# Performance work log

Hardware: AMD Instinct MI355X
Metric: run time of the kernel (lower is better)

## Reference

```python
import jax, jax.numpy as jnp
import numpy as np

N = 50000      # nodes
E = 800000     # edges (avg degree 16)
IN = 256       # in_ft
F1, F2, F3 = 128, 128, 256  # out_ft_list


def _p(k, shape):
    return jax.random.normal(k, shape, dtype=jnp.float32) * 0.05


def setup_inputs() -> dict:
    key = jax.random.key(0)
    ks = jax.random.split(key, 14)
    return {
        "x": jax.random.normal(ks[0], (N, IN), dtype=jnp.float32),
        "edge_index": jax.random.randint(ks[1], (2, E), 0, N, dtype=jnp.int64),
        # proj Linear
        "Wp": _p(ks[2], (IN, F1)), "bp": jnp.zeros((F1,), jnp.float32),
        # SAGEConv1: lin_l (on aggregated neighbors, carries bias) + lin_r (root)
        "Wl1": _p(ks[3], (IN, F1)), "bl1": jnp.zeros((F1,), jnp.float32), "Wr1": _p(ks[4], (IN, F1)),
        # SAGEConv2: input is concat(x_p, h1) -> 2*F1
        "Wl2": _p(ks[5], (2 * F1, F2)), "bl2": jnp.zeros((F2,), jnp.float32), "Wr2": _p(ks[6], (2 * F1, F2)),
        # SAGEConv3: input is concat(x_p, h1, h2) -> 2*F1 + F2
        "Wl3": _p(ks[7], (2 * F1 + F2, F3)), "bl3": jnp.zeros((F3,), jnp.float32), "Wr3": _p(ks[8], (2 * F1 + F2, F3)),
    }


def _sage_mean(h, src, dst, Wl, bl, Wr):
    # PyG SAGEConv(aggr='mean'): out = lin_l(mean_{j in N(i)} h_j) + lin_r(h_i)
    msg = h[src]                                              # [E, F_in]
    summed = jax.ops.segment_sum(msg, dst, num_segments=N)    # [N, F_in]
    deg = jax.ops.segment_sum(jnp.ones((src.shape[0],), h.dtype), dst, num_segments=N)
    mean = summed / jnp.maximum(deg, 1.0)[:, None]
    return mean @ Wl + bl + h @ Wr


def reference(x, edge_index, Wp, bp, Wl1, bl1, Wr1, Wl2, bl2, Wr2, Wl3, bl3, Wr3):
    src, dst = edge_index[0], edge_index[1]  # messages flow src -> dst
    act = jax.nn.relu
    # dropout p=0 (eval) -> identity
    x_p = act(x @ Wp + bp)                                    # [N, F1]
    h1 = act(_sage_mean(x, src, dst, Wl1, bl1, Wr1))          # [N, F1]
    in2 = jnp.concatenate([x_p, h1], axis=1)                  # [N, 2*F1]
    h2 = act(_sage_mean(in2, src, dst, Wl2, bl2, Wr2))        # [N, F2]
    in3 = jnp.concatenate([x_p, h1, h2], axis=1)              # [N, 2*F1+F2]
    h3 = act(_sage_mean(in3, src, dst, Wl3, bl3, Wr3))        # [N, F3]
    return h3
```

## Files before the change

kernel.cpp:

```cpp
#include <hip/hip_runtime.h>

#define MAXDEG 64

typedef _Float16 f16x8 __attribute__((ext_vector_type(8)));
typedef _Float16 f16x4 __attribute__((ext_vector_type(4)));
typedef _Float16 f16x2 __attribute__((ext_vector_type(2)));
typedef float f32x4 __attribute__((ext_vector_type(4)));

struct Blk {
  void* p;
  int mode;
  int relu;
  int ld;
  int c0;
};
struct Epi { Blk b[4]; };


__global__ void build_ell_kernel(const int* __restrict__ ei, int E,
                                 int* __restrict__ deg, int* __restrict__ ell) {
  int e = blockIdx.x * blockDim.x + threadIdx.x;
  if (e >= E) return;
  int s = ei[e];
  int d = ei[E + e];
  int slot = atomicAdd(&deg[d], 1);
  if (slot < MAXDEG) ell[d * MAXDEG + slot] = s;
}

__global__ void invdeg_kernel(const int* __restrict__ deg, float* __restrict__ inv, int N) {
  int i = blockIdx.x * blockDim.x + threadIdx.x;
  if (i < N) inv[i] = 1.0f / (float)(deg[i] > 1 ? deg[i] : 1);
}


__global__ void pack_kernel(const float* __restrict__ Wp, const float* __restrict__ Wl1,
                            const float* __restrict__ Wr1, const float* __restrict__ Wl2,
                            const float* __restrict__ Wr2, const float* __restrict__ Wl3,
                            const float* __restrict__ Wr3,
                            const float* __restrict__ bp, const float* __restrict__ bl1,
                            const float* __restrict__ bl2, const float* __restrict__ bl3,
                            _Float16* __restrict__ Bt1, _Float16* __restrict__ Bt2,
                            _Float16* __restrict__ Bt3,
                            float* __restrict__ bias1, float* __restrict__ bias2,
                            float* __restrict__ bias3) {
  int i = blockIdx.x * blockDim.x + threadIdx.x;
  if (i < 384 * 256) {
    int c = i / 256, k = i % 256;
    float v;
    if (c < 128) v = Wp[k * 128 + c];
    else if (c < 256) v = Wl1[k * 128 + (c - 128)];
    else v = Wr1[k * 128 + (c - 256)];
    Bt1[(long)c * 256 + k] = (_Float16)v;
  }
  if (i < 256 * 256) {
    int c = i / 256, k = i % 256;
    float v = (c < 128) ? Wl2[k * 128 + c] : Wr2[k * 128 + (c - 128)];
    Bt2[(long)c * 256 + k] = (_Float16)v;
  }
  if (i < 512 * 384) {
    int c = i / 384, k = i % 384;
    float v = (c < 256) ? Wl3[k * 256 + c] : Wr3[k * 256 + (c - 256)];
    Bt3[(long)c * 384 + k] = (_Float16)v;
  }
  if (i < 384) bias1[i] = (i < 128) ? bp[i] : ((i < 256) ? 0.f : bl1[i - 256]);
  if (i < 256) bias2[i] = (i < 128) ? 0.f : bl2[i - 128];
  if (i < 512) bias3[i] = (i < 256) ? 0.f : bl3[i - 256];
}


__global__ __launch_bounds__(256)
void convert_kernel(const float* __restrict__ src, long n4, _Float16* __restrict__ dst) {
  long i = (long)blockIdx.x * 256 + threadIdx.x;
  if (i >= n4) return;
  float4 v = *(const float4*)(src + i * 4);
  f16x4 h;
  h[0] = (_Float16)v.x; h[1] = (_Float16)v.y;
  h[2] = (_Float16)v.z; h[3] = (_Float16)v.w;
  *(f16x4*)(dst + i * 4) = h;
}


__global__ __launch_bounds__(256)
void gemm_mfma(const _Float16* __restrict__ A, int lda, int K, int M,
               const _Float16* __restrict__ Bt, int ldb,
               const float* __restrict__ bias,
               const _Float16* __restrict__ zbuf, Epi epi, int ncol) {
  __shared__ _Float16 As[128 * 64];
  __shared__ _Float16 Bs[128 * 64];
  const int t = threadIdx.x;
  const int lane = t & 63;
  const int w = t >> 6;
  const int wr = w >> 1, wc = w & 1;

  int g = blockIdx.x, total = gridDim.x;
  int xcd = g & 7, idx = g >> 3;
  int q8 = total >> 3, r8 = total & 7;
  int logical = (xcd < r8 ? xcd * (q8 + 1) : r8 * (q8 + 1) + (xcd - r8) * q8) + idx;
  int bx = logical / ncol, by = logical - bx * ncol;

  const int row0 = bx * 128;
  const int col0 = by * 128;

  f32x4 acc[4][4];
#pragma unroll
  for (int m = 0; m < 4; m++)
#pragma unroll
    for (int n = 0; n < 4; n++)
#pragma unroll
      for (int j = 0; j < 4; j++) acc[m][n][j] = 0.f;

  const _Float16* srcA[4];
  const _Float16* srcB[4];
  int liveA[4];
  _Float16* ldsA[4];
  _Float16* ldsB[4];
#pragma unroll
  for (int q = 0; q < 4; q++) {
    int s = w * 4 + q;
    int rl = s * 8 + (lane >> 3);
    int c = lane & 7;
    int cs = c ^ (rl & 7);
    long ra = (long)row0 + rl;
    liveA[q] = (ra < M) ? 1 : 0;
    srcA[q] = liveA[q] ? (A + ra * lda + (cs << 3)) : zbuf;
    srcB[q] = Bt + ((long)col0 + rl) * ldb + (cs << 3);
    ldsA[q] = &As[s * 512];
    ldsB[q] = &Bs[s * 512];
  }

  int arow[4], brow[4];
#pragma unroll
  for (int m = 0; m < 4; m++) arow[m] = wr * 64 + m * 16 + (lane & 15);
#pragma unroll
  for (int n = 0; n < 4; n++) brow[n] = wc * 64 + n * 16 + (lane & 15);

  for (int kb = 0; kb < K; kb += 64) {
#pragma unroll
    for (int q = 0; q < 4; q++) {
      const _Float16* pa = srcA[q] + (liveA[q] ? kb : 0);
      __builtin_amdgcn_global_load_lds(
          (const __attribute__((address_space(1))) unsigned int*)pa,
          (__attribute__((address_space(3))) unsigned int*)ldsA[q], 16, 0, 0);
      const _Float16* pb = srcB[q] + kb;
      __builtin_amdgcn_global_load_lds(
          (const __attribute__((address_space(1))) unsigned int*)pb,
          (__attribute__((address_space(3))) unsigned int*)ldsB[q], 16, 0, 0);
    }
    __syncthreads();
#pragma unroll
    for (int kk = 0; kk < 2; kk++) {
      f16x8 af[4], bfr[4];
      int cc = kk * 4 + (lane >> 4);
#pragma unroll
      for (int m = 0; m < 4; m++) {
        int r = arow[m];
        af[m] = *(const f16x8*)&As[r * 64 + ((cc ^ (r & 7)) << 3)];
      }
#pragma unroll
      for (int n = 0; n < 4; n++) {
        int r = brow[n];
        bfr[n] = *(const f16x8*)&Bs[r * 64 + ((cc ^ (r & 7)) << 3)];
      }
#pragma unroll
      for (int m = 0; m < 4; m++)
#pragma unroll
        for (int n = 0; n < 4; n++)
          acc[m][n] = __builtin_amdgcn_mfma_f32_16x16x32_f16(af[m], bfr[n], acc[m][n], 0, 0, 0);
    }
    __syncthreads();
  }

  Blk bk = epi.b[by];
  float bb[4];
#pragma unroll
  for (int n = 0; n < 4; n++) bb[n] = bias[col0 + wc * 64 + n * 16 + (lane & 15)];

#pragma unroll
  for (int m = 0; m < 4; m++) {
#pragma unroll
    for (int j = 0; j < 4; j++) {
      int r = row0 + wr * 64 + m * 16 + (lane >> 4) * 4 + j;
      if (r >= M) continue;
      long base = (long)r * bk.ld + bk.c0 + wc * 64 + (lane & 15);
#pragma unroll
      for (int n = 0; n < 4; n++) {
        float v = acc[m][n][j] + bb[n];
        if (bk.relu) v = fmaxf(v, 0.f);
        if (bk.mode == 0) {
          ((float*)bk.p)[base + n * 16] = v;
        } else {
          ((_Float16*)bk.p)[base + n * 16] = (_Float16)v;
        }
      }
    }
  }
}


template <int V>
__global__ __launch_bounds__(256)
void gather_kernel(const int* __restrict__ ell, const int* __restrict__ deg,
                   const float* __restrict__ inv,
                   const _Float16* __restrict__ y, int yld,
                   const float* __restrict__ z, int zld, int zc,
                   _Float16* __restrict__ oh, int ohLd, int ohC,
                   float* __restrict__ of, int ofLd, int ofC, int N) {
  int wid = (blockIdx.x * blockDim.x + threadIdx.x) >> 6;
  int lane = threadIdx.x & 63;
  if (wid >= N) return;
  int d = deg[wid];
  if (d > MAXDEG) d = MAXDEG;
  float s[V];
#pragma unroll
  for (int v = 0; v < V; v++) s[v] = 0.f;
  const int* el = ell + wid * MAXDEG;
  const int off = lane * V;
  int e = 0;
  for (; e + 4 <= d; e += 4) {
    const _Float16* p0 = y + (size_t)el[e] * yld + off;
    const _Float16* p1 = y + (size_t)el[e + 1] * yld + off;
    const _Float16* p2 = y + (size_t)el[e + 2] * yld + off;
    const _Float16* p3 = y + (size_t)el[e + 3] * yld + off;
    if (V == 2) {
      f16x2 a = *(const f16x2*)p0, b = *(const f16x2*)p1;
      f16x2 c = *(const f16x2*)p2, dd = *(const f16x2*)p3;
#pragma unroll
      for (int v = 0; v < 2; v++)
        s[v] += ((float)a[v] + (float)b[v]) + ((float)c[v] + (float)dd[v]);
    } else {
      f16x4 a = *(const f16x4*)p0, b = *(const f16x4*)p1;
      f16x4 c = *(const f16x4*)p2, dd = *(const f16x4*)p3;
#pragma unroll
      for (int v = 0; v < 4; v++)
        s[v] += ((float)a[v] + (float)b[v]) + ((float)c[v] + (float)dd[v]);
    }
  }
  for (; e < d; e++) {
    const _Float16* p0 = y + (size_t)el[e] * yld + off;
    if (V == 2) {
      f16x2 a = *(const f16x2*)p0;
#pragma unroll
      for (int v = 0; v < 2; v++) s[v] += (float)a[v];
    } else {
      f16x4 a = *(const f16x4*)p0;
#pragma unroll
      for (int v = 0; v < 4; v++) s[v] += (float)a[v];
    }
  }
  float sc = inv[wid];
  float h[V];
  const float* zp = z + (size_t)wid * zld + zc + off;
#pragma unroll
  for (int v = 0; v < V; v++) h[v] = fmaxf(fmaf(s[v], sc, zp[v]), 0.f);
  if (of) {
    float* op = of + (size_t)wid * ofLd + ofC + off;
    if (V == 2) {
      float2 w2; w2.x = h[0]; w2.y = h[1];
      *(float2*)op = w2;
    } else {
      float4 w4; w4.x = h[0]; w4.y = h[1]; w4.z = h[2]; w4.w = h[3];
      *(float4*)op = w4;
    }
  }
  if (oh) {
    _Float16* ap = oh + (size_t)wid * ohLd + ohC + off;
    if (V == 2) {
      f16x2 hh;
      hh[0] = (_Float16)h[0]; hh[1] = (_Float16)h[1];
      *(f16x2*)ap = hh;
    } else {
      f16x4 hh;
      hh[0] = (_Float16)h[0]; hh[1] = (_Float16)h[1];
      hh[2] = (_Float16)h[2]; hh[3] = (_Float16)h[3];
      *(f16x4*)ap = hh;
    }
  }
}


extern "C" void kernel_launch(void* const* d_in, const int* in_sizes, int n_in,
                              void* d_out, int out_size, void* d_ws, size_t ws_size,
                              hipStream_t stream) {
  const float* x   = (const float*)d_in[0];
  const int*   ei  = (const int*)d_in[1];
  const float* Wp  = (const float*)d_in[2];
  const float* bp  = (const float*)d_in[3];
  const float* Wl1 = (const float*)d_in[4];
  const float* bl1 = (const float*)d_in[5];
  const float* Wr1 = (const float*)d_in[6];
  const float* Wl2 = (const float*)d_in[7];
  const float* bl2 = (const float*)d_in[8];
  const float* Wr2 = (const float*)d_in[9];
  const float* Wl3 = (const float*)d_in[10];
  const float* bl3 = (const float*)d_in[11];
  const float* Wr3 = (const float*)d_in[12];
  float* out = (float*)d_out;

  const int N = in_sizes[0] / 256;
  const int E = in_sizes[1] / 2;

  char* ws = (char*)d_ws;
  size_t off = 0;
  auto carve = [&](size_t bytes) -> char* {
    char* p = ws + off;
    off = (off + bytes + 255) & ~(size_t)255;
    return p;
  };
  _Float16* A1    = (_Float16*)carve((size_t)N * 256 * 2);
  float*    z2    = (float*)A1;
  _Float16* A23   = (_Float16*)carve((size_t)N * 384 * 2);
  _Float16* ybuf  = (_Float16*)carve((size_t)N * 256 * 2);
  float*    z1    = (float*)carve((size_t)N * 128 * 4);
  int*      deg   = (int*)carve((size_t)N * 4);
  float*    inv   = (float*)carve((size_t)N * 4);
  int*      ell   = (int*)carve((size_t)N * MAXDEG * 4);
  _Float16* Bt1   = (_Float16*)carve((size_t)384 * 256 * 2);
  _Float16* Bt2   = (_Float16*)carve((size_t)256 * 256 * 2);
  _Float16* Bt3   = (_Float16*)carve((size_t)512 * 384 * 2);
  float*    bias1 = (float*)carve(384 * 4);
  float*    bias2 = (float*)carve(256 * 4);
  float*    bias3 = (float*)carve(512 * 4);
  _Float16* zbuf  = (_Float16*)carve(256);
  if (off > ws_size) return;

  hipMemsetAsync(deg, 0, (size_t)N * 4, stream);
  hipMemsetAsync(zbuf, 0, 256, stream);
  build_ell_kernel<<<(E + 255) / 256, 256, 0, stream>>>(ei, E, deg, ell);
  invdeg_kernel<<<(N + 255) / 256, 256, 0, stream>>>(deg, inv, N);
  pack_kernel<<<(512 * 384 + 255) / 256, 256, 0, stream>>>(
      Wp, Wl1, Wr1, Wl2, Wr2, Wl3, Wr3, bp, bl1, bl2, bl3,
      Bt1, Bt2, Bt3, bias1, bias2, bias3);

  const int MBG = (N + 127) / 128;
  const int gblocks = (N + 3) / 4;

  convert_kernel<<<(int)(((long)N * 64 + 255) / 256), 256, 0, stream>>>(x, (long)N * 64, A1);
  Epi e1;
  e1.b[0] = { A23,  1, 1, 384, 0 };
  e1.b[1] = { ybuf, 1, 0, 128, 0 };
  e1.b[2] = { z1,   0, 0, 128, 0 };
  e1.b[3] = { nullptr, 0, 0, 0, 0 };
  gemm_mfma<<<MBG * 3, 256, 0, stream>>>(A1, 256, 256, N, Bt1, 256, bias1, zbuf, e1, 3);
  gather_kernel<2><<<gblocks, 256, 0, stream>>>(ell, deg, inv, ybuf, 128, z1, 128, 0,
                                                A23, 384, 128, nullptr, 0, 0, N);

  Epi e2;
  e2.b[0] = { ybuf, 1, 0, 128, 0 };
  e2.b[1] = { z2,   0, 0, 128, 0 };
  e2.b[2] = { nullptr, 0, 0, 0, 0 };
  e2.b[3] = { nullptr, 0, 0, 0, 0 };
  gemm_mfma<<<MBG * 2, 256, 0, stream>>>(A23, 384, 256, N, Bt2, 256, bias2, zbuf, e2, 2);
  gather_kernel<2><<<gblocks, 256, 0, stream>>>(ell, deg, inv, ybuf, 128, z2, 128, 0,
                                                A23, 384, 256, nullptr, 0, 0, N);

  Epi e3;
  e3.b[0] = { ybuf, 1, 0, 256, 0   };
  e3.b[1] = { ybuf, 1, 0, 256, 128 };
  e3.b[2] = { out,  0, 0, 256, 0   };
  e3.b[3] = { out,  0, 0, 256, 128 };
  gemm_mfma<<<MBG * 4, 256, 0, stream>>>(A23, 384, 384, N, Bt3, 384, bias3, zbuf, e3, 4);
  gather_kernel<4><<<gblocks, 256, 0, stream>>>(ell, deg, inv, ybuf, 256, out, 256, 0,
                                                nullptr, 0, 0, out, 256, 0, N);
}
```

Before: 423.6 us.

## Use fp16 root-term buffers and packed fp16 neighbor accumulation in gather

```diff
diff --git a/kernel.cpp b/kernel.cpp
--- a/kernel.cpp
+++ b/kernel.cpp
@@ -202,56 +202,49 @@
 void gather_kernel(const int* __restrict__ ell, const int* __restrict__ deg,
                    const float* __restrict__ inv,
                    const _Float16* __restrict__ y, int yld,
-                   const float* __restrict__ z, int zld, int zc,
+                   const _Float16* __restrict__ zh, int zld, int zc,
                    _Float16* __restrict__ oh, int ohLd, int ohC,
                    float* __restrict__ of, int ofLd, int ofC, int N) {
+  typedef _Float16 f16v __attribute__((ext_vector_type(V)));
   int wid = (blockIdx.x * blockDim.x + threadIdx.x) >> 6;
   int lane = threadIdx.x & 63;
   if (wid >= N) return;
   int d = deg[wid];
   if (d > MAXDEG) d = MAXDEG;
-  float s[V];
-#pragma unroll
-  for (int v = 0; v < V; v++) s[v] = 0.f;
   const int* el = ell + wid * MAXDEG;
   const int off = lane * V;
+
+  f16v acc = (f16v)(_Float16)0.f;
   int e = 0;
+  for (; e + 8 <= d; e += 8) {
+    f16v r0 = *(const f16v*)(y + (size_t)el[e + 0] * yld + off);
+    f16v r1 = *(const f16v*)(y + (size_t)el[e + 1] * yld + off);
+    f16v r2 = *(const f16v*)(y + (size_t)el[e + 2] * yld + off);
+    f16v r3 = *(const f16v*)(y + (size_t)el[e + 3] * yld + off);
+    f16v r4 = *(const f16v*)(y + (size_t)el[e + 4] * yld + off);
+    f16v r5 = *(const f16v*)(y + (size_t)el[e + 5] * yld + off);
+    f16v r6 = *(const f16v*)(y + (size_t)el[e + 6] * yld + off);
+    f16v r7 = *(const f16v*)(y + (size_t)el[e + 7] * yld + off);
+    acc += ((r0 + r1) + (r2 + r3)) + ((r4 + r5) + (r6 + r7));
+  }
   for (; e + 4 <= d; e += 4) {
-    const _Float16* p0 = y + (size_t)el[e] * yld + off;
-    const _Float16* p1 = y + (size_t)el[e + 1] * yld + off;
-    const _Float16* p2 = y + (size_t)el[e + 2] * yld + off;
-    const _Float16* p3 = y + (size_t)el[e + 3] * yld + off;
-    if (V == 2) {
-      f16x2 a = *(const f16x2*)p0, b = *(const f16x2*)p1;
-      f16x2 c = *(const f16x2*)p2, dd = *(const f16x2*)p3;
-#pragma unroll
-      for (int v = 0; v < 2; v++)
-        s[v] += ((float)a[v] + (float)b[v]) + ((float)c[v] + (float)dd[v]);
-    } else {
-      f16x4 a = *(const f16x4*)p0, b = *(const f16x4*)p1;
-      f16x4 c = *(const f16x4*)p2, dd = *(const f16x4*)p3;
-#pragma unroll
-      for (int v = 0; v < 4; v++)
-        s[v] += ((float)a[v] + (float)b[v]) + ((float)c[v] + (float)dd[v]);
-    }
+    f16v r0 = *(const f16v*)(y + (size_t)el[e + 0] * yld + off);
+    f16v r1 = *(const f16v*)(y + (size_t)el[e + 1] * yld + off);
+    f16v r2 = *(const f16v*)(y + (size_t)el[e + 2] * yld + off);
+    f16v r3 = *(const f16v*)(y + (size_t)el[e + 3] * yld + off);
+    acc += (r0 + r1) + (r2 + r3);
   }
   for (; e < d; e++) {
-    const _Float16* p0 = y + (size_t)el[e] * yld + off;
-    if (V == 2) {
-      f16x2 a = *(const f16x2*)p0;
-#pragma unroll
-      for (int v = 0; v < 2; v++) s[v] += (float)a[v];
-    } else {
-      f16x4 a = *(const f16x4*)p0;
-#pragma unroll
-      for (int v = 0; v < 4; v++) s[v] += (float)a[v];
-    }
-  }
+    acc += *(const f16v*)(y + (size_t)el[e] * yld + off);
+  }
+
   float sc = inv[wid];
+  f16v zv = *(const f16v*)(zh + (size_t)wid * zld + zc + off);
   float h[V];
-  const float* zp = z + (size_t)wid * zld + zc + off;
-#pragma unroll
-  for (int v = 0; v < V; v++) h[v] = fmaxf(fmaf(s[v], sc, zp[v]), 0.f);
+#pragma unroll
+  for (int v = 0; v < V; v++)
+    h[v] = fmaxf(fmaf((float)acc[v], sc, (float)zv[v]), 0.f);
+
   if (of) {
     float* op = of + (size_t)wid * ofLd + ofC + off;
     if (V == 2) {
@@ -264,16 +257,10 @@
   }
   if (oh) {
     _Float16* ap = oh + (size_t)wid * ohLd + ohC + off;
-    if (V == 2) {
-      f16x2 hh;
-      hh[0] = (_Float16)h[0]; hh[1] = (_Float16)h[1];
-      *(f16x2*)ap = hh;
-    } else {
-      f16x4 hh;
-      hh[0] = (_Float16)h[0]; hh[1] = (_Float16)h[1];
-      hh[2] = (_Float16)h[2]; hh[3] = (_Float16)h[3];
-      *(f16x4*)ap = hh;
-    }
+    f16v hh;
+#pragma unroll
+    for (int v = 0; v < V; v++) hh[v] = (_Float16)h[v];
+    *(f16v*)ap = hh;
   }
 }
 
@@ -307,10 +294,11 @@
     return p;
   };
   _Float16* A1    = (_Float16*)carve((size_t)N * 256 * 2);
-  float*    z2    = (float*)A1;
+  _Float16* z2    = A1;
+  _Float16* z3    = A1;
   _Float16* A23   = (_Float16*)carve((size_t)N * 384 * 2);
   _Float16* ybuf  = (_Float16*)carve((size_t)N * 256 * 2);
-  float*    z1    = (float*)carve((size_t)N * 128 * 4);
+  _Float16* z1    = (_Float16*)carve((size_t)N * 128 * 2);
   int*      deg   = (int*)carve((size_t)N * 4);
   float*    inv   = (float*)carve((size_t)N * 4);
   int*      ell   = (int*)carve((size_t)N * MAXDEG * 4);
@@ -338,7 +326,7 @@
   Epi e1;
   e1.b[0] = { A23,  1, 1, 384, 0 };
   e1.b[1] = { ybuf, 1, 0, 128, 0 };
-  e1.b[2] = { z1,   0, 0, 128, 0 };
+  e1.b[2] = { z1,   1, 0, 128, 0 };
   e1.b[3] = { nullptr, 0, 0, 0, 0 };
   gemm_mfma<<<MBG * 3, 256, 0, stream>>>(A1, 256, 256, N, Bt1, 256, bias1, zbuf, e1, 3);
   gather_kernel<2><<<gblocks, 256, 0, stream>>>(ell, deg, inv, ybuf, 128, z1, 128, 0,
@@ -346,7 +334,7 @@
 
   Epi e2;
   e2.b[0] = { ybuf, 1, 0, 128, 0 };
-  e2.b[1] = { z2,   0, 0, 128, 0 };
+  e2.b[1] = { z2,   1, 0, 128, 0 };
   e2.b[2] = { nullptr, 0, 0, 0, 0 };
   e2.b[3] = { nullptr, 0, 0, 0, 0 };
   gemm_mfma<<<MBG * 2, 256, 0, stream>>>(A23, 384, 256, N, Bt2, 256, bias2, zbuf, e2, 2);
@@ -356,9 +344,9 @@
   Epi e3;
   e3.b[0] = { ybuf, 1, 0, 256, 0   };
   e3.b[1] = { ybuf, 1, 0, 256, 128 };
-  e3.b[2] = { out,  0, 0, 256, 0   };
-  e3.b[3] = { out,  0, 0, 256, 128 };
+  e3.b[2] = { z3,   1, 0, 256, 0   };
+  e3.b[3] = { z3,   1, 0, 256, 128 };
   gemm_mfma<<<MBG * 4, 256, 0, stream>>>(A23, 384, 384, N, Bt3, 384, bias3, zbuf, e3, 4);
-  gather_kernel<4><<<gblocks, 256, 0, stream>>>(ell, deg, inv, ybuf, 256, out, 256, 0,
+  gather_kernel<4><<<gblocks, 256, 0, stream>>>(ell, deg, inv, ybuf, 256, z3, 256, 0,
                                                 nullptr, 0, 0, out, 256, 0, N);
 }
```

Measured after the change: 407.1 us. -3.9%, faster.
